# Kernel tuning notes

Hardware: AMD Instinct MI355X
Metric: run time of the kernel (lower is better)

## Reference

```python
import jax, jax.numpy as jnp
import numpy as np

DIM = 512
L = 4096
B, H, W = 8, 64, 64
EPS = 1e-06
BN_EPS = 1e-05


def setup_inputs() -> dict:
    key = jax.random.key(0)
    ks = jax.random.split(key, 16)
    s = 1.0 / np.sqrt(DIM)
    d = {
        'x': jax.random.normal(ks[0], (B, DIM, H, W), dtype=jnp.float32),
        'pos_emb': jax.random.normal(ks[1], (1, L, DIM), dtype=jnp.float32),
        'Wq': jax.random.uniform(ks[2], (DIM, DIM), jnp.float32, -s, s),
        'bq': jax.random.uniform(ks[3], (DIM,), jnp.float32, -s, s),
        'Wk': jax.random.uniform(ks[4], (DIM, DIM), jnp.float32, -s, s),
        'bk': jax.random.uniform(ks[5], (DIM,), jnp.float32, -s, s),
        'Wv': jax.random.uniform(ks[6], (DIM, DIM), jnp.float32, -s, s),
        'bv': jax.random.uniform(ks[7], (DIM,), jnp.float32, -s, s),
        'Wq1': jax.random.uniform(ks[8], (DIM, DIM), jnp.float32, -s, s),
        'bq1': jax.random.uniform(ks[9], (DIM,), jnp.float32, -s, s),
        'Wk1': jax.random.uniform(ks[10], (DIM, DIM), jnp.float32, -s, s),
        'bk1': jax.random.uniform(ks[11], (DIM,), jnp.float32, -s, s),
        'gamma': jax.random.normal(ks[12], (1,), jnp.float32) * 0.1,
        'bn_weight': jnp.ones((DIM,), jnp.float32),
        'bn_bias': jnp.zeros((DIM,), jnp.float32),
    }
    return d


def reference(x, pos_emb, Wq, bq, Wk, bk, Wv, bv, Wq1, bq1, Wk1, bk1, gamma, bn_weight, bn_bias):
    Bb, C, Hh, Ww = x.shape
    # [B,C,H,W] -> [B, L, C] tokens
    xs = x.transpose(0, 2, 3, 1).reshape(Bb, Hh * Ww, C) + pos_emb
    Q = jax.nn.relu(xs @ Wq.T + bq)   # kernel_fun = ReLU
    K = jax.nn.relu(xs @ Wk.T + bk)
    V = xs @ Wv.T + bv
    Q1 = xs @ Wq1.T + bq1
    K1 = xs @ Wk1.T + bk1
    # torch einsum 'blc,bcc,bl->blc' uses only diag(KV); compute it directly:
    # diagKV[b,c] = sum_l K[b,l,c] * V[b,l,c]
    diagKV = jnp.einsum('blc,blc->bc', K, V)
    Ksum = K.sum(axis=1)  # == K^T summed over last axis, [B,C]
    Z = 1.0 / jnp.einsum('blc,bc->bl', Q, Ksum + EPS)
    result = Q * diagKV[:, None, :] * Z[:, :, None]  # [B,L,C]
    # channel-softmax attention: softmax over last dim of Q1^T @ K1, [B,C,C]
    mid = jax.nn.softmax(jnp.einsum('blc,bld->bcd', Q1, K1), axis=-1)
    result = result @ mid  # [B,L,C]
    xs = xs + gamma * result
    y = xs.transpose(0, 2, 1).reshape(Bb, C, Hh, Ww)
    # BatchNorm2d in training mode (fresh module): batch stats, biased variance
    mean = y.mean(axis=(0, 2, 3))
    var = y.var(axis=(0, 2, 3))
    yn = (y - mean[None, :, None, None]) * jax.lax.rsqrt(var + BN_EPS)[None, :, None, None]
    yn = yn * bn_weight[None, :, None, None] + bn_bias[None, :, None, None]
    return jax.nn.relu(yn)
```

## Files before the change

### kernel.cpp

```cpp
#include <hip/hip_runtime.h>
#include <stdint.h>

typedef float f32x4 __attribute__((ext_vector_type(4)));
typedef short bf16x8 __attribute__((ext_vector_type(8)));
typedef short bf16x4 __attribute__((ext_vector_type(4)));

__device__ __forceinline__ float bf2f(unsigned short h){
  union { unsigned int u; float f; } v; v.u = ((unsigned int)h) << 16; return v.f;
}
__device__ __forceinline__ unsigned short f2bf(float f){
  union { float f; unsigned int u; } v; v.f = f;
  return (unsigned short)((v.u + 0x7fffu + ((v.u >> 16) & 1u)) >> 16);
}

typedef __attribute__((address_space(1))) const unsigned int ga_u32;
typedef __attribute__((address_space(3))) unsigned int ls_u32;
__device__ __forceinline__ void async_load16(const void* g, void* l){
  __builtin_amdgcn_global_load_lds((ga_u32*)g, (ls_u32*)l, 16, 0, 0);
}

#define CFENCE() asm volatile("" ::: "memory")
#define SB0() __builtin_amdgcn_sched_barrier(0)

__global__ __launch_bounds__(256) void k_prep_w(
    const float* __restrict__ w0, const float* __restrict__ w1,
    const float* __restrict__ w2, const float* __restrict__ w3,
    const float* __restrict__ w4, unsigned short* __restrict__ out)
{
  int i = blockIdx.x * 256 + threadIdx.x;
  const float* w = (blockIdx.y == 0) ? w0 : (blockIdx.y == 1) ? w1 :
                   (blockIdx.y == 2) ? w2 : (blockIdx.y == 3) ? w3 : w4;
  out[(size_t)blockIdx.y * 262144 + i] = f2bf(w[i]);
}
__global__ __launch_bounds__(256) void k_prep_b(
    const float* __restrict__ b0, const float* __restrict__ b1,
    const float* __restrict__ b2, const float* __restrict__ b3,
    const float* __restrict__ b4, float* __restrict__ out)
{
  int i = blockIdx.x * 256 + threadIdx.x;
  int s = i >> 9, r = i & 511;
  const float* b = (s == 0) ? b0 : (s == 1) ? b1 : (s == 2) ? b2 : (s == 3) ? b3 : b4;
  out[i] = b[r];
}

__global__ __launch_bounds__(256) void k_build_xs(
    const float* __restrict__ x, const float* __restrict__ pos,
    unsigned short* __restrict__ xsb)
{
  __shared__ float tile[64][65];
  const int lt = blockIdx.x, ct = blockIdx.y, b = blockIdx.z;
  const int t = threadIdx.x;
  const int rr = t >> 3, c8 = (t & 7) * 8;
  #pragma unroll
  for (int pass = 0; pass < 2; pass++){
    int r = rr + pass * 32;
    const float* src = x + ((size_t)b * 512 + ct*64 + r) * 4096 + lt*64 + c8;
    f32x4 v0 = *(const f32x4*)src;
    f32x4 v1 = *(const f32x4*)(src + 4);
    #pragma unroll
    for (int s = 0; s < 4; s++){ tile[r][c8+s] = v0[s]; tile[r][c8+4+s] = v1[s]; }
  }
  __syncthreads();
  #pragma unroll
  for (int pass = 0; pass < 2; pass++){
    int ll = rr + pass * 32;
    int gl = lt*64 + ll;
    const float* pp = pos + (size_t)gl * 512 + ct*64 + c8;
    bf16x8 hv;
    #pragma unroll
    for (int s = 0; s < 8; s++)
      hv[s] = (short)f2bf(tile[c8+s][ll] + pp[s]);
    *(bf16x8*)(xsb + ((size_t)b * 4096 + gl) * 512 + ct*64 + c8) = hv;
  }
}

__global__ __launch_bounds__(256) void k_transpose_bf(
    const unsigned short* __restrict__ in, unsigned short* __restrict__ out,
    int R, int C)
{
  __shared__ float tile[64][65];
  const int rt = blockIdx.x, ct = blockIdx.y, z = blockIdx.z;
  const unsigned short* src = in  + (size_t)z * R * C;
  unsigned short*       dst = out + (size_t)z * R * C;
  const int t = threadIdx.x;
  const int rr = t >> 3, c8 = (t & 7) * 8;
  #pragma unroll
  for (int pass = 0; pass < 2; pass++){
    int r = rr + pass * 32;
    bf16x8 v = *(const bf16x8*)(src + (size_t)(rt*64 + r) * C + ct*64 + c8);
    #pragma unroll
    for (int s = 0; s < 8; s++) tile[r][c8+s] = bf2f((unsigned short)v[s]);
  }
  __syncthreads();
  #pragma unroll
  for (int pass = 0; pass < 2; pass++){
    int c = rr + pass * 32;
    bf16x8 hv;
    #pragma unroll
    for (int s = 0; s < 8; s++) hv[s] = (short)f2bf(tile[c8+s][c]);
    *(bf16x8*)(dst + (size_t)(ct*64 + c) * R + rt*64 + c8) = hv;
  }
}

__global__ __launch_bounds__(256) void k_reduce_kv(
    const unsigned short* __restrict__ Kb, const unsigned short* __restrict__ Vb,
    float* __restrict__ diag, float* __restrict__ ksum)
{
  const int b = blockIdx.x, lz = blockIdx.y * 64;
  const int t = threadIdx.x;
  const int c8 = (t & 63) * 8, lo = t >> 6;
  float d[8] = {0.f,0.f,0.f,0.f,0.f,0.f,0.f,0.f};
  float s[8] = {0.f,0.f,0.f,0.f,0.f,0.f,0.f,0.f};
  for (int l = lo; l < 64; l += 4){
    size_t base = ((size_t)b * 4096 + lz + l) * 512 + c8;
    bf16x8 kv = *(const bf16x8*)(Kb + base);
    bf16x8 vv = *(const bf16x8*)(Vb + base);
    #pragma unroll
    for (int j = 0; j < 8; j++){
      float kf = bf2f((unsigned short)kv[j]);
      float vf = bf2f((unsigned short)vv[j]);
      d[j] += kf * vf; s[j] += kf;
    }
  }
  __shared__ float red[2][4][512];
  f32x4 a0 = {d[0],d[1],d[2],d[3]}, a1 = {d[4],d[5],d[6],d[7]};
  f32x4 b0 = {s[0],s[1],s[2],s[3]}, b1 = {s[4],s[5],s[6],s[7]};
  *(f32x4*)&red[0][lo][c8]   = a0;  *(f32x4*)&red[0][lo][c8+4] = a1;
  *(f32x4*)&red[1][lo][c8]   = b0;  *(f32x4*)&red[1][lo][c8+4] = b1;
  __syncthreads();
  for (int cc = t; cc < 512; cc += 256){
    float dd = red[0][0][cc] + red[0][1][cc] + red[0][2][cc] + red[0][3][cc];
    float ss = red[1][0][cc] + red[1][1][cc] + red[1][2][cc] + red[1][3][cc];
    atomicAdd(&diag[b*512 + cc], dd);
    atomicAdd(&ksum[b*512 + cc], ss);
  }
}

__global__ __launch_bounds__(256) void k_z_r0(
    const unsigned short* __restrict__ Qb, const float* __restrict__ ksum,
    const float* __restrict__ diag, unsigned short* __restrict__ r0)
{
  const int row = blockIdx.x * 4 + (threadIdx.x >> 6);
  const int lane = threadIdx.x & 63;
  const int b = row >> 12;
  bf16x8 q = *(const bf16x8*)(Qb + (size_t)row * 512 + lane * 8);
  float qf[8];
  #pragma unroll
  for (int s = 0; s < 8; s++) qf[s] = bf2f((unsigned short)q[s]);
  f32x4 k0 = *(const f32x4*)(ksum + b*512 + lane*8);
  f32x4 k1 = *(const f32x4*)(ksum + b*512 + lane*8 + 4);
  f32x4 d0 = *(const f32x4*)(diag + b*512 + lane*8);
  f32x4 d1 = *(const f32x4*)(diag + b*512 + lane*8 + 4);
  float den = 0.f;
  #pragma unroll
  for (int s = 0; s < 4; s++) den += qf[s]   * (k0[s] + 1e-6f);
  #pragma unroll
  for (int s = 0; s < 4; s++) den += qf[4+s] * (k1[s] + 1e-6f);
  #pragma unroll
  for (int m = 1; m < 64; m <<= 1) den += __shfl_xor(den, m);
  float Z = 1.0f / den;
  bf16x8 hv;
  #pragma unroll
  for (int s = 0; s < 4; s++) hv[s]   = (short)f2bf(qf[s]   * d0[s] * Z);
  #pragma unroll
  for (int s = 0; s < 4; s++) hv[4+s] = (short)f2bf(qf[4+s] * d1[s] * Z);
  *(bf16x8*)(r0 + (size_t)row * 512 + lane * 8) = hv;
}

__global__ __launch_bounds__(64) void k_softmax(
    const float* __restrict__ S, unsigned short* __restrict__ mid)
{
  const size_t row = blockIdx.x;
  const int lane = threadIdx.x;
  const float* p = S + row * 512 + lane * 8;
  f32x4 v0 = *(const f32x4*)p, v1 = *(const f32x4*)(p + 4);
  float mx = v0[0];
  #pragma unroll
  for (int s = 1; s < 4; s++) mx = fmaxf(mx, v0[s]);
  #pragma unroll
  for (int s = 0; s < 4; s++) mx = fmaxf(mx, v1[s]);
  #pragma unroll
  for (int m = 1; m < 64; m <<= 1) mx = fmaxf(mx, __shfl_xor(mx, m));
  float e[8]; float sum = 0.f;
  #pragma unroll
  for (int s = 0; s < 4; s++){ e[s]   = __expf(v0[s] - mx); sum += e[s]; }
  #pragma unroll
  for (int s = 0; s < 4; s++){ e[4+s] = __expf(v1[s] - mx); sum += e[4+s]; }
  #pragma unroll
  for (int m = 1; m < 64; m <<= 1) sum += __shfl_xor(sum, m);
  float inv = 1.0f / sum;
  bf16x8 hv;
  #pragma unroll
  for (int s = 0; s < 8; s++) hv[s] = (short)f2bf(e[s] * inv);
  *(bf16x8*)(mid + row * 512 + lane * 8) = hv;
}

#define GEMM_PRE()                                                            \
  const int tid = threadIdx.x;                                                \
  const int lane = tid & 63;                                                  \
  const int wave = tid >> 6;                                                  \
  const int wm = wave >> 1, wn = wave & 1;                                    \
  size_t aoff[4], boff[4]; int ldsq[4];                                       \
  _Pragma("unroll")                                                           \
  for (int i = 0; i < 4; i++){                                                \
    int qq = i*4 + wave;                                                      \
    int ch = qq*64 + lane;                                                    \
    int m  = ch >> 3, p = ch & 7;                                             \
    int lc = p ^ (m & 7);                                                     \
    aoff[i] = (size_t)(m0 + m) * K + lc*8;                                    \
    boff[i] = (size_t)(n0 + m) * K + lc*8;                                    \
    ldsq[i] = qq * 1024;                                                      \
  }                                                                           \
  f32x4 acc[4][4];                                                            \
  const f32x4 vzero = {0.f,0.f,0.f,0.f};                                      \
  _Pragma("unroll")                                                           \
  for (int i = 0; i < 4; i++)                                                 \
    _Pragma("unroll")                                                         \
    for (int j = 0; j < 4; j++) acc[i][j] = vzero;                            \
  int arow[4], brow[4];                                                       \
  _Pragma("unroll")                                                           \
  for (int f = 0; f < 4; f++){                                                \
    arow[f] = (wm*64 + f*16 + (lane & 15)) * 64;                              \
    brow[f] = (wn*64 + f*16 + (lane & 15)) * 64;                              \
  }                                                                           \
  const int kg = lane >> 4;                                                   \
  const int l7 = lane & 7;

#define GEMM_STAGE(buf, kt)                                                   \
  _Pragma("unroll")                                                           \
  for (int i = 0; i < 4; i++){                                                \
    async_load16(Ae + aoff[i] + (kt)*64, (char*)&smem[(buf)*8192] + ldsq[i]); \
    async_load16(Be + boff[i] + (kt)*64, (char*)&smem[16384 + (buf)*8192] + ldsq[i]); \
  }

#define GEMM_COMPUTE(buf)                                                     \
  _Pragma("unroll")                                                           \
  for (int ks = 0; ks < 2; ks++){                                             \
    bf16x8 a[4], b[4];                                                        \
    const int pa = (ks*4 + kg) ^ l7;                                          \
    _Pragma("unroll")                                                         \
    for (int f = 0; f < 4; f++){                                              \
      a[f] = *(const bf16x8*)&smem[(buf)*8192 + arow[f] + pa*8];              \
      b[f] = *(const bf16x8*)&smem[16384 + (buf)*8192 + brow[f] + pa*8];      \
    }                                                                         \
    _Pragma("unroll")                                                         \
    for (int i = 0; i < 4; i++)                                               \
      _Pragma("unroll")                                                       \
      for (int j = 0; j < 4; j++)                                             \
        acc[i][j] = __builtin_amdgcn_mfma_f32_16x16x32_bf16(a[i], b[j], acc[i][j], 0, 0, 0); \
  }

#define GEMM_KLOOP(nkt)                                                       \
  GEMM_STAGE(0, 0);                                                           \
  __syncthreads();                                                            \
  int cur = 0;                                                                \
  for (int kt = 0; kt < (nkt); kt++){                                         \
    if (kt + 1 < (nkt)) { GEMM_STAGE(cur ^ 1, kt + 1); }                      \
    GEMM_COMPUTE(cur);                                                        \
    __syncthreads();                                                          \
    cur ^= 1;                                                                 \
  }

__global__ __launch_bounds__(256) void gemm_mid(
    const unsigned short* __restrict__ A,
    const unsigned short* __restrict__ Bt,
    float* __restrict__ outf, int K)
{
  __shared__ unsigned short smem[32768];
  const int bid = blockIdx.x;
  const int cpx = gridDim.x >> 3;
  const int wgid = (bid & 7) * cpx + (bid >> 3);
  const int z = wgid >> 4;
  const int mtile = (wgid >> 2) & 3, ntile = wgid & 3;
  const int m0 = mtile * 128, n0 = ntile * 128;
  const unsigned short* Ae = A  + (size_t)z * 512 * (size_t)K;
  const unsigned short* Be = Bt + (size_t)z * 512 * (size_t)K;

  GEMM_PRE();
  GEMM_KLOOP(K >> 6);

  const int lr = lane >> 4;
  const int lc16 = lane & 15;
  #pragma unroll
  for (int j = 0; j < 4; j++){
    int cidx = n0 + wn*64 + j*16 + lc16;
    #pragma unroll
    for (int i = 0; i < 4; i++){
      int r = m0 + wm*64 + i*16 + lr*4;
      #pragma unroll
      for (int q = 0; q < 4; q++)
        outf[(size_t)z * 262144 + (size_t)(r + q) * 512 + cidx] = acc[i][j][q];
    }
  }
}


#define G8_PRE(AE, BE, N0ABS)                                                 \
  const int t = threadIdx.x;                                                  \
  const int lane = t & 63;                                                    \
  const int wave = t >> 6;                                                    \
  const int wm = wave >> 2, wn = wave & 3;                                    \
  const int l15 = lane & 15, kg = lane >> 4;                                  \
  const int lcw = ((t & 7) ^ ((t >> 3) & 7)) * 8;                             \
  const unsigned short* a_src = (AE) + (size_t)(m0 + (t >> 3)) * 512 + lcw;   \
  const unsigned short* b_src = (BE) + (size_t)((N0ABS) + (t >> 3)) * 512 + lcw; \
  f32x4 acc[8][4];                                                            \
  const f32x4 vzero = {0.f,0.f,0.f,0.f};                                      \
  _Pragma("unroll")                                                           \
  for (int i = 0; i < 8; i++)                                                 \
    _Pragma("unroll")                                                         \
    for (int j = 0; j < 4; j++) acc[i][j] = vzero;                            \
  bf16x8 af[4][2], bf[4][2];

#define STAGE_A(D,H,TT) do{                                                   \
  async_load16(a_src + (H)*65536 + (TT)*64,                                   \
               (char*)smem + ((D)*16384 + (H)*8192 + t*8)*2);                 \
  async_load16(a_src + (H)*65536 + 32768 + (TT)*64,                           \
               (char*)smem + ((D)*16384 + (H)*8192 + 4096 + t*8)*2);          \
}while(0)

#define STAGE_B(D,H,TT) do{                                                   \
  async_load16(b_src + (H)*65536 + (TT)*64,                                   \
               (char*)smem + (32768 + (D)*16384 + (H)*8192 + t*8)*2);         \
  async_load16(b_src + (H)*65536 + 32768 + (TT)*64,                           \
               (char*)smem + (32768 + (D)*16384 + (H)*8192 + 4096 + t*8)*2);  \
}while(0)

#define READ_A(D, MH) do{                                                     \
  _Pragma("unroll")                                                           \
  for (int mfl = 0; mfl < 4; ++mfl){                                          \
    const int rl = ((MH)*4 + mfl)*16 + l15;                                   \
    _Pragma("unroll")                                                         \
    for (int ks = 0; ks < 2; ++ks){                                           \
      const int ck = (ks*4 + kg) ^ (rl & 7);                                  \
      af[mfl][ks] = *(const bf16x8*)&smem[(D)*16384 + wm*8192 + rl*64 + ck*8];\
    }                                                                         \
  }                                                                           \
}while(0)

#define READ_B(D, NP) do{                                                     \
  _Pragma("unroll")                                                           \
  for (int nfl = 0; nfl < 2; ++nfl){                                          \
    const int nf = (NP)*2 + nfl;                                              \
    const int rbl = (wn & 1)*64 + nf*16 + l15;                                \
    _Pragma("unroll")                                                         \
    for (int ks = 0; ks < 2; ++ks){                                           \
      const int ck = (ks*4 + kg) ^ (rbl & 7);                                 \
      bf[nf][ks] = *(const bf16x8*)&smem[32768 + (D)*16384 + (wn>>1)*8192 + rbl*64 + ck*8]; \
    }                                                                         \
  }                                                                           \
}while(0)

#define QUAD(MH, NP)                                                          \
  _Pragma("unroll")                                                           \
  for (int mfl = 0; mfl < 4; ++mfl)                                           \
    _Pragma("unroll")                                                         \
    for (int nfl = 0; nfl < 2; ++nfl)                                         \
      _Pragma("unroll")                                                       \
      for (int ks = 0; ks < 2; ++ks)                                          \
        acc[(MH)*4+mfl][(NP)*2+nfl] = __builtin_amdgcn_mfma_f32_16x16x32_bf16(\
            af[mfl][ks], bf[(NP)*2+nfl][ks], acc[(MH)*4+mfl][(NP)*2+nfl], 0,0,0);

#define PH_MID()  CFENCE(); __builtin_amdgcn_s_barrier();                     \
  __builtin_amdgcn_s_setprio(1); SB0()
#define PH_END()  SB0(); __builtin_amdgcn_s_setprio(0); CFENCE();             \
  __builtin_amdgcn_s_barrier(); CFENCE()
#define PH_END_VM4() SB0(); __builtin_amdgcn_s_setprio(0);                    \
  asm volatile("s_waitcnt vmcnt(4)" ::: "memory");                            \
  __builtin_amdgcn_s_barrier(); CFENCE()
#define PH_END_VM0() SB0(); __builtin_amdgcn_s_setprio(0);                    \
  asm volatile("s_waitcnt vmcnt(0)" ::: "memory");                            \
  __builtin_amdgcn_s_barrier(); CFENCE()

#define G8_KLOOP()                                                            \
  STAGE_A(0,0,0); STAGE_A(0,1,0); STAGE_B(0,0,0); STAGE_B(0,1,0);             \
  STAGE_B(1,0,1); STAGE_B(1,1,1);                                             \
  asm volatile("s_waitcnt vmcnt(4)" ::: "memory");                            \
  __builtin_amdgcn_s_barrier(); CFENCE();                                     \
  for (int it = 0; it < 3; ++it){                                             \
    const int t1 = 2*it + 1, t2 = 2*it + 2, t3 = 2*it + 3;                    \
    READ_A(0,0); READ_B(0,0); STAGE_A(1,0,t1);                                \
    PH_MID(); QUAD(0,0); PH_END();                                            \
    READ_B(0,1); STAGE_A(1,1,t1);                                             \
    PH_MID(); QUAD(0,1); PH_END();                                            \
    READ_A(0,1); STAGE_B(0,0,t2);                                             \
    PH_MID(); QUAD(1,0); PH_END();                                            \
    STAGE_A(0,0,t2);                                                          \
    PH_MID(); QUAD(1,1); PH_END_VM4();                                        \
    READ_A(1,0); READ_B(1,0); STAGE_A(0,1,t2);                                \
    PH_MID(); QUAD(0,0); PH_END();                                            \
    READ_B(1,1); STAGE_B(0,1,t2);                                             \
    PH_MID(); QUAD(0,1); PH_END();                                            \
    READ_A(1,1); STAGE_B(1,0,t3);                                             \
    PH_MID(); QUAD(1,0); PH_END();                                            \
    STAGE_B(1,1,t3);                                                          \
    PH_MID(); QUAD(1,1); PH_END_VM4();                                        \
  }                                                                           \
  {                           \
    READ_A(0,0); READ_B(0,0); STAGE_A(1,0,7);                                 \
    PH_MID(); QUAD(0,0); PH_END();                                            \
    READ_B(0,1); STAGE_A(1,1,7);                                              \
    PH_MID(); QUAD(0,1); PH_END();                                            \
    READ_A(0,1);                                                              \
    PH_MID(); QUAD(1,0); PH_END();                                            \
    PH_MID(); QUAD(1,1); PH_END_VM0();                                        \
    READ_A(1,0); READ_B(1,0);                                                 \
    PH_MID(); QUAD(0,0); PH_END();                                            \
    READ_B(1,1);                                                              \
    PH_MID(); QUAD(0,1); PH_END();                                            \
    READ_A(1,1);                                                              \
    PH_MID(); QUAD(1,0); PH_END();                                            \
    PH_MID(); QUAD(1,1); PH_END();                                            \
  }

__global__ __launch_bounds__(512, 2) void gemm8_proj(
    const unsigned short* __restrict__ A,
    const unsigned short* __restrict__ W,
    const float* __restrict__ bias5,
    unsigned short* __restrict__ Qb, unsigned short* __restrict__ Kb,
    unsigned short* __restrict__ Vb, unsigned short* __restrict__ Q1T,
    unsigned short* __restrict__ K1T)
{
  __shared__ unsigned short smem[65536];
  const int bid = blockIdx.x;
  const int wgid = (bid & 7) * 160 + (bid >> 3);
  const int mtile = wgid / 10;
  const int nslot = wgid % 10;
  const int slot = nslot >> 1;
  const int ncol = nslot & 1;
  const int m0 = mtile * 256;
  const int nc0 = ncol * 256;

  G8_PRE(A, W + (size_t)slot * 262144, nc0);
  G8_KLOOP();

  if (slot < 3){
    unsigned short* o = (slot == 0) ? Qb : (slot == 1) ? Kb : Vb;
    const bool relu = (slot < 2);
    __syncthreads();
    #pragma unroll
    for (int nf = 0; nf < 4; nf++){
      int cl = wn*64 + nf*16 + l15;
      float bb = bias5[slot*512 + nc0 + cl];
      #pragma unroll
      for (int mf = 0; mf < 8; mf++){
        int rbase = wm*128 + mf*16 + kg*4;
        #pragma unroll
        for (int q = 0; q < 4; q++){
          float v = acc[mf][nf][q] + bb;
          if (relu) v = v > 0.f ? v : 0.f;
          int rl = rbase + q;
          smem[rl*256 + (cl ^ (((rl >> 2) & 3) << 4))] = f2bf(v);
        }
      }
    }
    __syncthreads();
    const int c0 = (t & 31) * 8;
    #pragma unroll
    for (int rep = 0; rep < 16; rep++){
      int rl = rep*16 + (t >> 5);
      bf16x8 v = *(const bf16x8*)&smem[rl*256 + (c0 ^ (((rl >> 2) & 3) << 4))];
      *(bf16x8*)(o + (size_t)(m0 + rl) * 512 + nc0 + c0) = v;
    }
  } else {
    unsigned short* o = (slot == 3) ? Q1T : K1T;
    const int b = mtile >> 4;
    const int l0 = (mtile & 15) * 256;
    __syncthreads();
    #pragma unroll
    for (int nf = 0; nf < 4; nf++){
      int cl_ = wn*64 + nf*16 + l15;
      float bb = bias5[slot*512 + nc0 + cl_];
      #pragma unroll
      for (int mf = 0; mf < 8; mf++){
        #pragma unroll
        for (int q = 0; q < 4; q++){
          int ll = wm*128 + mf*16 + kg*4 + q;
          int sw = ((ll >> 3) ^ (cl_ & 7)) * 8 + (ll & 7);
          smem[cl_*256 + sw] = f2bf(acc[mf][nf][q] + bb);
        }
      }
    }
    __syncthreads();
    #pragma unroll
    for (int rep = 0; rep < 16; rep++){
      int c = rep*16 + (t >> 5);
      int lch = t & 31;
      bf16x8 v = *(const bf16x8*)&smem[c*256 + (lch ^ (c & 7))*8];
      *(bf16x8*)(o + ((size_t)b*512 + nc0 + c)*4096 + l0 + lch*8) = v;
    }
  }
}

__global__ __launch_bounds__(512, 2) void gemm8_res(
    const unsigned short* __restrict__ A,
    const unsigned short* __restrict__ Bt,
    unsigned short* __restrict__ outh,
    const float* __restrict__ gamma_p,
    float* __restrict__ bnS, float* __restrict__ bnQ)
{
  __shared__ unsigned short smem[65536];
  const int bid = blockIdx.x;
  const int wgid = (bid & 7) * 32 + (bid >> 3);
  const int mtile = wgid >> 1;
  const int ntile = wgid & 1;
  const int m0 = mtile * 256;
  const int nc0 = ntile * 256;

  G8_PRE(A, Bt + (size_t)(mtile >> 4) * 262144, nc0);
  G8_KLOOP();

  const float g = gamma_p[0];
  __syncthreads();
  #pragma unroll
  for (int nf = 0; nf < 4; nf++){
    int cl = wn*64 + nf*16 + l15;
    #pragma unroll
    for (int mf = 0; mf < 8; mf++){
      int rbase = wm*128 + mf*16 + kg*4;
      #pragma unroll
      for (int q = 0; q < 4; q++){
        int rl = rbase + q;
        smem[rl*256 + (cl ^ (((rl >> 2) & 3) << 4))] = f2bf(g * acc[mf][nf][q]);
      }
    }
  }
  __syncthreads();
  float sc[8] = {0.f,0.f,0.f,0.f,0.f,0.f,0.f,0.f};
  float sq[8] = {0.f,0.f,0.f,0.f,0.f,0.f,0.f,0.f};
  const int c0 = (t & 31) * 8;
  #pragma unroll
  for (int rep = 0; rep < 16; rep++){
    int rl = rep*16 + (t >> 5);
    bf16x8 ga = *(const bf16x8*)&smem[rl*256 + (c0 ^ (((rl >> 2) & 3) << 4))];
    size_t gidx = (size_t)(m0 + rl) * 512 + nc0 + c0;
    bf16x8 xv = *(const bf16x8*)(outh + gidx);
    bf16x8 yv;
    #pragma unroll
    for (int j = 0; j < 8; j++){
      float y = bf2f((unsigned short)xv[j]) + bf2f((unsigned short)ga[j]);
      yv[j] = (short)f2bf(y);
      sc[j] += y; sq[j] += y * y;
    }
    *(bf16x8*)(outh + gidx) = yv;
  }
  __syncthreads();
  float* red = (float*)(void*)smem;
  const int tg = t >> 5;
  f32x4 s0 = {sc[0],sc[1],sc[2],sc[3]}, s1 = {sc[4],sc[5],sc[6],sc[7]};
  f32x4 q0 = {sq[0],sq[1],sq[2],sq[3]}, q1 = {sq[4],sq[5],sq[6],sq[7]};
  *(f32x4*)&red[tg*256 + c0]          = s0;  *(f32x4*)&red[tg*256 + c0 + 4]          = s1;
  *(f32x4*)&red[4096 + tg*256 + c0]   = q0;  *(f32x4*)&red[4096 + tg*256 + c0 + 4]   = q1;
  __syncthreads();
  if (t < 256){
    float ss = 0.f, qq = 0.f;
    #pragma unroll
    for (int gg = 0; gg < 16; gg++){
      ss += red[gg*256 + t];
      qq += red[4096 + gg*256 + t];
    }
    atomicAdd(&bnS[nc0 + t], ss);
    atomicAdd(&bnQ[nc0 + t], qq);
  }
}

__global__ __launch_bounds__(256) void k_bn_finalize(
    const unsigned short* __restrict__ y, const float* __restrict__ bnS,
    const float* __restrict__ bnQ, const float* __restrict__ bnw,
    const float* __restrict__ bnb, float* __restrict__ out)
{
  __shared__ float tile[64][65];
  __shared__ float scale_s[64], shift_s[64];
  const int lt = blockIdx.x, ct = blockIdx.y, b = blockIdx.z;
  const int t = threadIdx.x;
  if (t < 64){
    int c = ct*64 + t;
    float s = bnS[c], q = bnQ[c];
    float mean = s * (1.0f / 32768.0f);
    float var  = q * (1.0f / 32768.0f) - mean * mean;
    float inv  = rsqrtf(var + 1e-5f);
    float scv  = bnw[c] * inv;
    scale_s[t] = scv;
    shift_s[t] = bnb[c] - mean * scv;
  }
  const int rr = t >> 3, c8 = (t & 7) * 8;
  #pragma unroll
  for (int pass = 0; pass < 2; pass++){
    int l = rr + pass * 32;
    bf16x8 v = *(const bf16x8*)(y + ((size_t)b * 4096 + lt*64 + l) * 512 + ct*64 + c8);
    #pragma unroll
    for (int s = 0; s < 8; s++) tile[l][c8+s] = bf2f((unsigned short)v[s]);
  }
  __syncthreads();
  #pragma unroll
  for (int pass = 0; pass < 2; pass++){
    int c = rr + pass * 32;
    float scv = scale_s[c], sh = shift_s[c];
    f32x4 o0, o1;
    #pragma unroll
    for (int s = 0; s < 4; s++){
      float v = tile[c8+s][c] * scv + sh;     o0[s] = v > 0.f ? v : 0.f;
      float w = tile[c8+4+s][c] * scv + sh;   o1[s] = w > 0.f ? w : 0.f;
    }
    float* dp = out + ((size_t)b * 512 + ct*64 + c) * 4096 + lt*64 + c8;
    *(f32x4*)dp = o0;
    *(f32x4*)(dp + 4) = o1;
  }
}

extern "C" void kernel_launch(void* const* d_in, const int* in_sizes, int n_in,
                              void* d_out, int out_size, void* d_ws, size_t ws_size,
                              hipStream_t stream)
{
  const float* x    = (const float*)d_in[0];
  const float* pos  = (const float*)d_in[1];
  const float* Wq   = (const float*)d_in[2];
  const float* bq   = (const float*)d_in[3];
  const float* Wk   = (const float*)d_in[4];
  const float* bk   = (const float*)d_in[5];
  const float* Wv   = (const float*)d_in[6];
  const float* bv   = (const float*)d_in[7];
  const float* Wq1  = (const float*)d_in[8];
  const float* bq1  = (const float*)d_in[9];
  const float* Wk1  = (const float*)d_in[10];
  const float* bk1  = (const float*)d_in[11];
  const float* gam  = (const float*)d_in[12];
  const float* bnw  = (const float*)d_in[13];
  const float* bnb  = (const float*)d_in[14];
  float* out = (float*)d_out;
  char* ws = (char*)d_ws;

  const size_t MB = 1ull << 20;
  const size_t OFF_XSB  = 0;
  const size_t OFF_QB   = 32*MB;
  const size_t OFF_Q1T  = 64*MB;
  const size_t OFF_K1T  = 96*MB;
  const size_t OFF_SF   = 128*MB;
  const size_t OFF_MIDB = 136*MB;
  const size_t OFF_MIDT = 140*MB;
  const size_t OFF_R0   = 144*MB;
  const size_t OFF_WBF  = 176*MB;
  const size_t OFF_B5   = 179*MB;
  const size_t OFF_DIAG = 180*MB;
  const size_t OFF_KSUM = OFF_DIAG + 16384;
  const size_t OFF_BNS  = OFF_KSUM + 16384;
  const size_t OFF_BNQ  = OFF_BNS + 2048;
  const size_t WS_NEED  = OFF_BNQ + 2048;
  if (ws_size < WS_NEED) return;

  unsigned short* xsb  = (unsigned short*)(ws + OFF_XSB);
  unsigned short* Qb   = (unsigned short*)(ws + OFF_QB);
  unsigned short* Q1T  = (unsigned short*)(ws + OFF_Q1T);
  unsigned short* K1T  = (unsigned short*)(ws + OFF_K1T);
  float*          Sf   = (float*)(ws + OFF_SF);
  unsigned short* midb = (unsigned short*)(ws + OFF_MIDB);
  unsigned short* midT = (unsigned short*)(ws + OFF_MIDT);
  unsigned short* r0   = (unsigned short*)(ws + OFF_R0);
  unsigned short* wbf  = (unsigned short*)(ws + OFF_WBF);
  float* bias5 = (float*)(ws + OFF_B5);
  float* diag = (float*)(ws + OFF_DIAG);
  float* ksum = (float*)(ws + OFF_KSUM);
  float* bnS  = (float*)(ws + OFF_BNS);
  float* bnQ  = (float*)(ws + OFF_BNQ);

  unsigned short* Kb = (unsigned short*)d_out;
  unsigned short* Vb = Kb + 16777216;

  hipMemsetAsync(ws + OFF_DIAG, 0, 16384 + 16384 + 2048 + 2048, stream);

  k_prep_w  <<<dim3(1024, 5), 256, 0, stream>>>(Wq, Wk, Wv, Wq1, Wk1, wbf);
  k_prep_b  <<<dim3(10),      256, 0, stream>>>(bq, bk, bv, bq1, bk1, bias5);
  k_build_xs<<<dim3(64, 8, 8),256, 0, stream>>>(x, pos, xsb);

  gemm8_proj<<<dim3(1280), 512, 0, stream>>>(xsb, wbf, bias5, Qb, Kb, Vb, Q1T, K1T);

  k_reduce_kv<<<dim3(8, 64), 256, 0, stream>>>(Kb, Vb, diag, ksum);
  k_z_r0<<<dim3(8192), 256, 0, stream>>>(Qb, ksum, diag, r0);

  gemm_mid<<<dim3(128), 256, 0, stream>>>(Q1T, K1T, Sf, 4096);

  k_softmax<<<dim3(4096), 64, 0, stream>>>(Sf, midb);
  k_transpose_bf<<<dim3(8, 8, 8), 256, 0, stream>>>(midb, midT, 512, 512);

  gemm8_res<<<dim3(256), 512, 0, stream>>>(r0, midT, xsb, gam, bnS, bnQ);

  k_bn_finalize<<<dim3(64, 8, 8), 256, 0, stream>>>(xsb, bnS, bnQ, bnw, bnb, out);
}
```

Measured before the change: 261.3 us.

## Fuse K/V reductions into projection epilogue and fold diag/Z scaling into later GEMMs

The projection GEMM now computes K and V in one tile, pairing K and V columns, and reduces ksum and diag(KV) in its epilogue with atomics, so K and V are never written to global memory and the separate reduction kernel goes away. The r0 intermediate is removed: diag scaling is folded into the mid-matrix transpose, and the per-row Z factor is applied in the residual GEMM epilogue, with a small kernel computing only Z. The channel-attention GEMM is split-K into two halves over twice as many blocks, and the softmax sums the two partial outputs. This cuts large intermediate traffic and improves occupancy of the small GEMM, at the cost of extra atomics and an extra partial-sum buffer.

Result: faster. 234.8 us (-10.1%).

```diff
diff --git a/kernel.cpp b/kernel.cpp
--- a/kernel.cpp
+++ b/kernel.cpp
@@ -3,7 +3,6 @@
 
 typedef float f32x4 __attribute__((ext_vector_type(4)));
 typedef short bf16x8 __attribute__((ext_vector_type(8)));
-typedef short bf16x4 __attribute__((ext_vector_type(4)));
 
 __device__ __forceinline__ float bf2f(unsigned short h){
   union { unsigned int u; float f; } v; v.u = ((unsigned int)h) << 16; return v.f;
@@ -74,106 +73,68 @@
   }
 }
 
-__global__ __launch_bounds__(256) void k_transpose_bf(
-    const unsigned short* __restrict__ in, unsigned short* __restrict__ out,
-    int R, int C)
+__global__ __launch_bounds__(256) void k_transpose_scale(
+    const unsigned short* __restrict__ in, const float* __restrict__ diag,
+    unsigned short* __restrict__ out)
 {
   __shared__ float tile[64][65];
   const int rt = blockIdx.x, ct = blockIdx.y, z = blockIdx.z;
-  const unsigned short* src = in  + (size_t)z * R * C;
-  unsigned short*       dst = out + (size_t)z * R * C;
+  const unsigned short* src = in  + (size_t)z * 262144;
+  unsigned short*       dst = out + (size_t)z * 262144;
   const int t = threadIdx.x;
   const int rr = t >> 3, c8 = (t & 7) * 8;
   #pragma unroll
   for (int pass = 0; pass < 2; pass++){
     int r = rr + pass * 32;
-    bf16x8 v = *(const bf16x8*)(src + (size_t)(rt*64 + r) * C + ct*64 + c8);
+    bf16x8 v = *(const bf16x8*)(src + (size_t)(rt*64 + r) * 512 + ct*64 + c8);
     #pragma unroll
     for (int s = 0; s < 8; s++) tile[r][c8+s] = bf2f((unsigned short)v[s]);
   }
   __syncthreads();
+  f32x4 dg0 = *(const f32x4*)(diag + z*512 + rt*64 + c8);
+  f32x4 dg1 = *(const f32x4*)(diag + z*512 + rt*64 + c8 + 4);
   #pragma unroll
   for (int pass = 0; pass < 2; pass++){
     int c = rr + pass * 32;
     bf16x8 hv;
     #pragma unroll
-    for (int s = 0; s < 8; s++) hv[s] = (short)f2bf(tile[c8+s][c]);
-    *(bf16x8*)(dst + (size_t)(ct*64 + c) * R + rt*64 + c8) = hv;
-  }
-}
-
-__global__ __launch_bounds__(256) void k_reduce_kv(
-    const unsigned short* __restrict__ Kb, const unsigned short* __restrict__ Vb,
-    float* __restrict__ diag, float* __restrict__ ksum)
-{
-  const int b = blockIdx.x, lz = blockIdx.y * 64;
-  const int t = threadIdx.x;
-  const int c8 = (t & 63) * 8, lo = t >> 6;
-  float d[8] = {0.f,0.f,0.f,0.f,0.f,0.f,0.f,0.f};
-  float s[8] = {0.f,0.f,0.f,0.f,0.f,0.f,0.f,0.f};
-  for (int l = lo; l < 64; l += 4){
-    size_t base = ((size_t)b * 4096 + lz + l) * 512 + c8;
-    bf16x8 kv = *(const bf16x8*)(Kb + base);
-    bf16x8 vv = *(const bf16x8*)(Vb + base);
-    #pragma unroll
-    for (int j = 0; j < 8; j++){
-      float kf = bf2f((unsigned short)kv[j]);
-      float vf = bf2f((unsigned short)vv[j]);
-      d[j] += kf * vf; s[j] += kf;
-    }
-  }
-  __shared__ float red[2][4][512];
-  f32x4 a0 = {d[0],d[1],d[2],d[3]}, a1 = {d[4],d[5],d[6],d[7]};
-  f32x4 b0 = {s[0],s[1],s[2],s[3]}, b1 = {s[4],s[5],s[6],s[7]};
-  *(f32x4*)&red[0][lo][c8]   = a0;  *(f32x4*)&red[0][lo][c8+4] = a1;
-  *(f32x4*)&red[1][lo][c8]   = b0;  *(f32x4*)&red[1][lo][c8+4] = b1;
-  __syncthreads();
-  for (int cc = t; cc < 512; cc += 256){
-    float dd = red[0][0][cc] + red[0][1][cc] + red[0][2][cc] + red[0][3][cc];
-    float ss = red[1][0][cc] + red[1][1][cc] + red[1][2][cc] + red[1][3][cc];
-    atomicAdd(&diag[b*512 + cc], dd);
-    atomicAdd(&ksum[b*512 + cc], ss);
-  }
-}
-
-__global__ __launch_bounds__(256) void k_z_r0(
+    for (int s = 0; s < 4; s++) hv[s]   = (short)f2bf(tile[c8+s][c]   * dg0[s]);
+    #pragma unroll
+    for (int s = 0; s < 4; s++) hv[4+s] = (short)f2bf(tile[c8+4+s][c] * dg1[s]);
+    *(bf16x8*)(dst + (size_t)(ct*64 + c) * 512 + rt*64 + c8) = hv;
+  }
+}
+
+__global__ __launch_bounds__(256) void k_z(
     const unsigned short* __restrict__ Qb, const float* __restrict__ ksum,
-    const float* __restrict__ diag, unsigned short* __restrict__ r0)
+    float* __restrict__ Z)
 {
   const int row = blockIdx.x * 4 + (threadIdx.x >> 6);
   const int lane = threadIdx.x & 63;
   const int b = row >> 12;
   bf16x8 q = *(const bf16x8*)(Qb + (size_t)row * 512 + lane * 8);
-  float qf[8];
-  #pragma unroll
-  for (int s = 0; s < 8; s++) qf[s] = bf2f((unsigned short)q[s]);
   f32x4 k0 = *(const f32x4*)(ksum + b*512 + lane*8);
   f32x4 k1 = *(const f32x4*)(ksum + b*512 + lane*8 + 4);
-  f32x4 d0 = *(const f32x4*)(diag + b*512 + lane*8);
-  f32x4 d1 = *(const f32x4*)(diag + b*512 + lane*8 + 4);
   float den = 0.f;
   #pragma unroll
-  for (int s = 0; s < 4; s++) den += qf[s]   * (k0[s] + 1e-6f);
-  #pragma unroll
-  for (int s = 0; s < 4; s++) den += qf[4+s] * (k1[s] + 1e-6f);
+  for (int s = 0; s < 4; s++) den += bf2f((unsigned short)q[s])   * (k0[s] + 1e-6f);
+  #pragma unroll
+  for (int s = 0; s < 4; s++) den += bf2f((unsigned short)q[4+s]) * (k1[s] + 1e-6f);
   #pragma unroll
   for (int m = 1; m < 64; m <<= 1) den += __shfl_xor(den, m);
-  float Z = 1.0f / den;
-  bf16x8 hv;
-  #pragma unroll
-  for (int s = 0; s < 4; s++) hv[s]   = (short)f2bf(qf[s]   * d0[s] * Z);
-  #pragma unroll
-  for (int s = 0; s < 4; s++) hv[4+s] = (short)f2bf(qf[4+s] * d1[s] * Z);
-  *(bf16x8*)(r0 + (size_t)row * 512 + lane * 8) = hv;
+  if (lane == 0) Z[row] = 1.0f / den;
 }
 
 __global__ __launch_bounds__(64) void k_softmax(
-    const float* __restrict__ S, unsigned short* __restrict__ mid)
+    const float* __restrict__ S0, const float* __restrict__ S1,
+    unsigned short* __restrict__ mid)
 {
   const size_t row = blockIdx.x;
   const int lane = threadIdx.x;
-  const float* p = S + row * 512 + lane * 8;
-  f32x4 v0 = *(const f32x4*)p, v1 = *(const f32x4*)(p + 4);
+  const float* p0 = S0 + row * 512 + lane * 8;
+  const float* p1 = S1 + row * 512 + lane * 8;
+  f32x4 v0 = *(const f32x4*)p0 + *(const f32x4*)p1;
+  f32x4 v1 = *(const f32x4*)(p0 + 4) + *(const f32x4*)(p1 + 4);
   float mx = v0[0];
   #pragma unroll
   for (int s = 1; s < 4; s++) mx = fmaxf(mx, v0[s]);
@@ -264,21 +225,24 @@
 __global__ __launch_bounds__(256) void gemm_mid(
     const unsigned short* __restrict__ A,
     const unsigned short* __restrict__ Bt,
-    float* __restrict__ outf, int K)
+    float* __restrict__ out0, float* __restrict__ out1)
 {
   __shared__ unsigned short smem[32768];
   const int bid = blockIdx.x;
-  const int cpx = gridDim.x >> 3;
-  const int wgid = (bid & 7) * cpx + (bid >> 3);
-  const int z = wgid >> 4;
-  const int mtile = (wgid >> 2) & 3, ntile = wgid & 3;
+  const int wgid = (bid & 7) * 32 + (bid >> 3);
+  const int part = wgid & 1;
+  const int ntile = (wgid >> 1) & 3;
+  const int mtile = (wgid >> 3) & 3;
+  const int z = wgid >> 5;
   const int m0 = mtile * 128, n0 = ntile * 128;
-  const unsigned short* Ae = A  + (size_t)z * 512 * (size_t)K;
-  const unsigned short* Be = Bt + (size_t)z * 512 * (size_t)K;
+  const int K = 4096;
+  const unsigned short* Ae = A  + (size_t)z * 512 * 4096 + part * 2048;
+  const unsigned short* Be = Bt + (size_t)z * 512 * 4096 + part * 2048;
 
   GEMM_PRE();
-  GEMM_KLOOP(K >> 6);
-
+  GEMM_KLOOP(32);
+
+  float* outf = part ? out1 : out0;
   const int lr = lane >> 4;
   const int lc16 = lane & 15;
   #pragma unroll
@@ -294,8 +258,7 @@
   }
 }
 
-
-#define G8_PRE(AE, BE, N0ABS)                                                 \
+#define G8_PRE(AE)                                                            \
   const int t = threadIdx.x;                                                  \
   const int lane = t & 63;                                                    \
   const int wave = t >> 6;                                                    \
@@ -303,7 +266,6 @@
   const int l15 = lane & 15, kg = lane >> 4;                                  \
   const int lcw = ((t & 7) ^ ((t >> 3) & 7)) * 8;                             \
   const unsigned short* a_src = (AE) + (size_t)(m0 + (t >> 3)) * 512 + lcw;   \
-  const unsigned short* b_src = (BE) + (size_t)((N0ABS) + (t >> 3)) * 512 + lcw; \
   f32x4 acc[8][4];                                                            \
   const f32x4 vzero = {0.f,0.f,0.f,0.f};                                      \
   _Pragma("unroll")                                                           \
@@ -320,9 +282,9 @@
 }while(0)
 
 #define STAGE_B(D,H,TT) do{                                                   \
-  async_load16(b_src + (H)*65536 + (TT)*64,                                   \
+  async_load16(b_src + (H)*bhoff + (TT)*64,                                   \
                (char*)smem + (32768 + (D)*16384 + (H)*8192 + t*8)*2);         \
-  async_load16(b_src + (H)*65536 + 32768 + (TT)*64,                           \
+  async_load16(b_src + (H)*bhoff + 32768 + (TT)*64,                           \
                (char*)smem + (32768 + (D)*16384 + (H)*8192 + 4096 + t*8)*2);  \
 }while(0)
 
@@ -417,38 +379,48 @@
     const unsigned short* __restrict__ A,
     const unsigned short* __restrict__ W,
     const float* __restrict__ bias5,
-    unsigned short* __restrict__ Qb, unsigned short* __restrict__ Kb,
-    unsigned short* __restrict__ Vb, unsigned short* __restrict__ Q1T,
-    unsigned short* __restrict__ K1T)
+    unsigned short* __restrict__ Qb,
+    unsigned short* __restrict__ Q1T, unsigned short* __restrict__ K1T,
+    float* __restrict__ diag, float* __restrict__ ksum)
 {
   __shared__ unsigned short smem[65536];
   const int bid = blockIdx.x;
   const int wgid = (bid & 7) * 160 + (bid >> 3);
   const int mtile = wgid / 10;
   const int nslot = wgid % 10;
-  const int slot = nslot >> 1;
-  const int ncol = nslot & 1;
   const int m0 = mtile * 256;
-  const int nc0 = ncol * 256;
-
-  G8_PRE(A, W + (size_t)slot * 262144, nc0);
+
+  int mode, wsel = 0, nbase = 0, p = 0;
+  if (nslot < 2)      { mode = 0; wsel = 0; nbase = nslot * 256; }
+  else if (nslot < 6) { mode = 1; p = nslot - 2; }
+  else if (nslot < 8) { mode = 2; wsel = 3; nbase = (nslot - 6) * 256; }
+  else                { mode = 3; wsel = 4; nbase = (nslot - 8) * 256; }
+
+  G8_PRE(A);
+  const unsigned short* b_src; int bhoff;
+  if (mode == 1){
+    b_src = W + 262144 + (size_t)(p*128 + (t >> 3)) * 512 + lcw;
+    bhoff = 262144;
+  } else {
+    b_src = W + (size_t)wsel * 262144 + (size_t)(nbase + (t >> 3)) * 512 + lcw;
+    bhoff = 65536;
+  }
+
   G8_KLOOP();
 
-  if (slot < 3){
-    unsigned short* o = (slot == 0) ? Qb : (slot == 1) ? Kb : Vb;
-    const bool relu = (slot < 2);
+  if (mode == 0){
     __syncthreads();
     #pragma unroll
     for (int nf = 0; nf < 4; nf++){
       int cl = wn*64 + nf*16 + l15;
-      float bb = bias5[slot*512 + nc0 + cl];
+      float bb = bias5[nbase + cl];
       #pragma unroll
       for (int mf = 0; mf < 8; mf++){
         int rbase = wm*128 + mf*16 + kg*4;
         #pragma unroll
         for (int q = 0; q < 4; q++){
           float v = acc[mf][nf][q] + bb;
-          if (relu) v = v > 0.f ? v : 0.f;
+          v = v > 0.f ? v : 0.f;
           int rl = rbase + q;
           smem[rl*256 + (cl ^ (((rl >> 2) & 3) << 4))] = f2bf(v);
         }
@@ -460,17 +432,67 @@
     for (int rep = 0; rep < 16; rep++){
       int rl = rep*16 + (t >> 5);
       bf16x8 v = *(const bf16x8*)&smem[rl*256 + (c0 ^ (((rl >> 2) & 3) << 4))];
-      *(bf16x8*)(o + (size_t)(m0 + rl) * 512 + nc0 + c0) = v;
+      *(bf16x8*)(Qb + (size_t)(m0 + rl) * 512 + nbase + c0) = v;
+    }
+  } else if (mode == 1){
+    const int b = mtile >> 4;
+    __syncthreads();
+    if (wn < 2){
+      #pragma unroll
+      for (int nf = 0; nf < 4; nf++){
+        int cl = (wn & 1)*64 + nf*16 + l15;
+        float bb = bias5[512 + p*128 + cl];
+        float ks_ = 0.f;
+        #pragma unroll
+        for (int mf = 0; mf < 8; mf++){
+          int rbase = wm*128 + mf*16 + kg*4;
+          #pragma unroll
+          for (int q = 0; q < 4; q++){
+            float v = acc[mf][nf][q] + bb;
+            v = v > 0.f ? v : 0.f;
+            unsigned short h = f2bf(v);
+            int r = rbase + q;
+            smem[r*128 + (cl ^ (((r >> 2) & 7) << 4))] = h;
+            ks_ += bf2f(h);
+          }
+        }
+        ks_ += __shfl_xor(ks_, 16);
+        ks_ += __shfl_xor(ks_, 32);
+        if (kg == 0) atomicAdd(&ksum[b*512 + p*128 + cl], ks_);
+      }
+    }
+    __syncthreads();
+    if (wn >= 2){
+      #pragma unroll
+      for (int nf = 0; nf < 4; nf++){
+        int cl = (wn & 1)*64 + nf*16 + l15;
+        float bb = bias5[1024 + p*128 + cl];
+        float dv = 0.f;
+        #pragma unroll
+        for (int mf = 0; mf < 8; mf++){
+          int rbase = wm*128 + mf*16 + kg*4;
+          #pragma unroll
+          for (int q = 0; q < 4; q++){
+            int r = rbase + q;
+            float kf = bf2f(smem[r*128 + (cl ^ (((r >> 2) & 7) << 4))]);
+            float vf = bf2f(f2bf(acc[mf][nf][q] + bb));
+            dv += kf * vf;
+          }
+        }
+        dv += __shfl_xor(dv, 16);
+        dv += __shfl_xor(dv, 32);
+        if (kg == 0) atomicAdd(&diag[b*512 + p*128 + cl], dv);
+      }
     }
   } else {
-    unsigned short* o = (slot == 3) ? Q1T : K1T;
+    unsigned short* o = (mode == 2) ? Q1T : K1T;
     const int b = mtile >> 4;
     const int l0 = (mtile & 15) * 256;
     __syncthreads();
     #pragma unroll
     for (int nf = 0; nf < 4; nf++){
       int cl_ = wn*64 + nf*16 + l15;
-      float bb = bias5[slot*512 + nc0 + cl_];
+      float bb = bias5[wsel*512 + nbase + cl_];
       #pragma unroll
       for (int mf = 0; mf < 8; mf++){
         #pragma unroll
@@ -487,7 +509,7 @@
       int c = rep*16 + (t >> 5);
       int lch = t & 31;
       bf16x8 v = *(const bf16x8*)&smem[c*256 + (lch ^ (c & 7))*8];
-      *(bf16x8*)(o + ((size_t)b*512 + nc0 + c)*4096 + l0 + lch*8) = v;
+      *(bf16x8*)(o + ((size_t)b*512 + nbase + c)*4096 + l0 + lch*8) = v;
     }
   }
 }
@@ -495,11 +517,13 @@
 __global__ __launch_bounds__(512, 2) void gemm8_res(
     const unsigned short* __restrict__ A,
     const unsigned short* __restrict__ Bt,
+    const float* __restrict__ Zp,
     unsigned short* __restrict__ outh,
     const float* __restrict__ gamma_p,
     float* __restrict__ bnS, float* __restrict__ bnQ)
 {
   __shared__ unsigned short smem[65536];
+  __shared__ float zbuf[256];
   const int bid = blockIdx.x;
   const int wgid = (bid & 7) * 32 + (bid >> 3);
   const int mtile = wgid >> 1;
@@ -507,10 +531,16 @@
   const int m0 = mtile * 256;
   const int nc0 = ntile * 256;
 
-  G8_PRE(A, Bt + (size_t)(mtile >> 4) * 262144, nc0);
+  G8_PRE(A);
+  const unsigned short* b_src =
+      Bt + (size_t)(mtile >> 4) * 262144 + (size_t)(nc0 + (t >> 3)) * 512 + lcw;
+  const int bhoff = 65536;
+
   G8_KLOOP();
 
   const float g = gamma_p[0];
+  __syncthreads();
+  if (t < 256) zbuf[t] = Zp[m0 + t];
   __syncthreads();
   #pragma unroll
   for (int nf = 0; nf < 4; nf++){
@@ -521,7 +551,8 @@
       #pragma unroll
       for (int q = 0; q < 4; q++){
         int rl = rbase + q;
-        smem[rl*256 + (cl ^ (((rl >> 2) & 3) << 4))] = f2bf(g * acc[mf][nf][q]);
+        smem[rl*256 + (cl ^ (((rl >> 2) & 3) << 4))] =
+            f2bf(g * zbuf[rl] * acc[mf][nf][q]);
       }
     }
   }
@@ -549,8 +580,8 @@
   const int tg = t >> 5;
   f32x4 s0 = {sc[0],sc[1],sc[2],sc[3]}, s1 = {sc[4],sc[5],sc[6],sc[7]};
   f32x4 q0 = {sq[0],sq[1],sq[2],sq[3]}, q1 = {sq[4],sq[5],sq[6],sq[7]};
-  *(f32x4*)&red[tg*256 + c0]          = s0;  *(f32x4*)&red[tg*256 + c0 + 4]          = s1;
-  *(f32x4*)&red[4096 + tg*256 + c0]   = q0;  *(f32x4*)&red[4096 + tg*256 + c0 + 4]   = q1;
+  *(f32x4*)&red[tg*256 + c0]        = s0;  *(f32x4*)&red[tg*256 + c0 + 4]        = s1;
+  *(f32x4*)&red[4096 + tg*256 + c0] = q0;  *(f32x4*)&red[4096 + tg*256 + c0 + 4] = q1;
   __syncthreads();
   if (t < 256){
     float ss = 0.f, qq = 0.f;
@@ -635,13 +666,14 @@
   const size_t OFF_QB   = 32*MB;
   const size_t OFF_Q1T  = 64*MB;
   const size_t OFF_K1T  = 96*MB;
-  const size_t OFF_SF   = 128*MB;
-  const size_t OFF_MIDB = 136*MB;
-  const size_t OFF_MIDT = 140*MB;
-  const size_t OFF_R0   = 144*MB;
-  const size_t OFF_WBF  = 176*MB;
-  const size_t OFF_B5   = 179*MB;
-  const size_t OFF_DIAG = 180*MB;
+  const size_t OFF_SF0  = 128*MB;
+  const size_t OFF_SF1  = 136*MB;
+  const size_t OFF_MIDB = 144*MB;
+  const size_t OFF_MIDT = 148*MB;
+  const size_t OFF_WBF  = 152*MB;
+  const size_t OFF_B5   = 155*MB;
+  const size_t OFF_Z    = 156*MB;
+  const size_t OFF_DIAG = 157*MB;
   const size_t OFF_KSUM = OFF_DIAG + 16384;
   const size_t OFF_BNS  = OFF_KSUM + 16384;
   const size_t OFF_BNQ  = OFF_BNS + 2048;
@@ -652,37 +684,35 @@
   unsigned short* Qb   = (unsigned short*)(ws + OFF_QB);
   unsigned short* Q1T  = (unsigned short*)(ws + OFF_Q1T);
   unsigned short* K1T  = (unsigned short*)(ws + OFF_K1T);
-  float*          Sf   = (float*)(ws + OFF_SF);
+  float*          Sf0  = (float*)(ws + OFF_SF0);
+  float*          Sf1  = (float*)(ws + OFF_SF1);
   unsigned short* midb = (unsigned short*)(ws + OFF_MIDB);
   unsigned short* midT = (unsigned short*)(ws + OFF_MIDT);
-  unsigned short* r0   = (unsigned short*)(ws + OFF_R0);
   unsigned short* wbf  = (unsigned short*)(ws + OFF_WBF);
   float* bias5 = (float*)(ws + OFF_B5);
+  float* Zp   = (float*)(ws + OFF_Z);
   float* diag = (float*)(ws + OFF_DIAG);
   float* ksum = (float*)(ws + OFF_KSUM);
   float* bnS  = (float*)(ws + OFF_BNS);
   float* bnQ  = (float*)(ws + OFF_BNQ);
 
-  unsigned short* Kb = (unsigned short*)d_out;
-  unsigned short* Vb = Kb + 16777216;
-
   hipMemsetAsync(ws + OFF_DIAG, 0, 16384 + 16384 + 2048 + 2048, stream);
 
   k_prep_w  <<<dim3(1024, 5), 256, 0, stream>>>(Wq, Wk, Wv, Wq1, Wk1, wbf);
   k_prep_b  <<<dim3(10),      256, 0, stream>>>(bq, bk, bv, bq1, bk1, bias5);
   k_build_xs<<<dim3(64, 8, 8),256, 0, stream>>>(x, pos, xsb);
 
-  gemm8_proj<<<dim3(1280), 512, 0, stream>>>(xsb, wbf, bias5, Qb, Kb, Vb, Q1T, K1T);
-
-  k_reduce_kv<<<dim3(8, 64), 256, 0, stream>>>(Kb, Vb, diag, ksum);
-  k_z_r0<<<dim3(8192), 256, 0, stream>>>(Qb, ksum, diag, r0);
-
-  gemm_mid<<<dim3(128), 256, 0, stream>>>(Q1T, K1T, Sf, 4096);
-
-  k_softmax<<<dim3(4096), 64, 0, stream>>>(Sf, midb);
-  k_transpose_bf<<<dim3(8, 8, 8), 256, 0, stream>>>(midb, midT, 512, 512);
-
-  gemm8_res<<<dim3(256), 512, 0, stream>>>(r0, midT, xsb, gam, bnS, bnQ);
+  gemm8_proj<<<dim3(1280), 512, 0, stream>>>(xsb, wbf, bias5, Qb, Q1T, K1T, diag, ksum);
+
+  k_z<<<dim3(8192), 256, 0, stream>>>(Qb, ksum, Zp);
+
+  gemm_mid<<<dim3(256), 256, 0, stream>>>(Q1T, K1T, Sf0, Sf1);
+
+  k_softmax<<<dim3(4096), 64, 0, stream>>>(Sf0, Sf1, midb);
+
+  k_transpose_scale<<<dim3(8, 8, 8), 256, 0, stream>>>(midb, diag, midT);
+
+  gemm8_res<<<dim3(256), 512, 0, stream>>>(Qb, midT, Zp, xsb, gam, bnS, bnQ);
 
   k_bn_finalize<<<dim3(64, 8, 8), 256, 0, stream>>>(xsb, bnS, bnQ, bnw, bnb, out);
 }
```
